# Kernel optimization log

Hardware: AMD Instinct MI355X
Metric: run time of the kernel (lower is better)

Reference implementation:

```python
import jax, jax.numpy as jnp
import numpy as np

SIZE, NC, BITS = 16, 3, 8
NV = NC * BITS * SIZE * SIZE  # 6144
NH = NV
N = 32
K_LS = 32   # fixed cap on T=0 local-search Gibbs sweeps (converged rows are fixed points)
K_CP = 16   # fixed cap on coupling MH iterations (converged rows masked out)


def float2bit(x, bits=BITS):
    # quantize [0,1) floats to `bits` binary planes, as in float2bit(...).flatten(1)
    q = jnp.clip(jnp.floor(x * (2 ** bits)), 0, 2 ** bits - 1).astype(jnp.int32)
    shifts = jnp.arange(bits, dtype=jnp.int32)
    b = (q[..., None] >> shifts) & 1  # [N,nc,H,W,bits]
    return b.astype(jnp.float32)


def energy(params, v, h0, h1):
    W0, W1, b0, b1, b2 = params
    e = -jnp.sum(v * b0, axis=1)
    e = e - jnp.sum(h0 * (v @ W0.T + b1), axis=1)
    e = e - jnp.sum(h1 * (h0 @ W1.T + b2), axis=1)
    return e


def _samp(logits, r, T):
    if T == 0:
        return (logits >= 0).astype(jnp.float32)
    return (r < jax.nn.sigmoid(logits / T)).astype(jnp.float32)


def gibbs_step(params, v, h0, h1, even, fix_v, T, key):
    W0, W1, b0, b1, b2 = params
    if T == 0:
        rv = rh0 = rh1 = None
    else:
        kv, k0, k1 = jax.random.split(key, 3)
        rv = jax.random.uniform(kv, v.shape)
        rh0 = jax.random.uniform(k0, h0.shape)
        rh1 = jax.random.uniform(k1, h1.shape)
    # 'even' sweep order: v -> odd h layers -> even h layers
    v_e = v if fix_v else _samp(h0 @ W0 + b0, rv, T)
    h1_e = _samp(h0 @ W1.T + b2, rh1, T)
    h0_e = _samp(v_e @ W0.T + b1 + h1_e @ W1, rh0, T)
    # 'odd' sweep order: even h layers -> v -> odd h layers
    h0_o = _samp(v @ W0.T + b1 + h1 @ W1, rh0, T)
    v_o = v if fix_v else _samp(h0_o @ W0 + b0, rv, T)
    h1_o = _samp(h0_o @ W1.T + b2, rh1, T)
    m = even[:, None]
    return (jnp.where(m, v_e, v_o), jnp.where(m, h0_e, h0_o), jnp.where(m, h1_e, h1_o))


def local_search(params, v, h0, h1, fix_v, key):
    # T=0 deterministic descent with a fixed per-row even/odd split (rand_u drawn once);
    # converged rows are fixed points of the map, so running a fixed K_LS sweeps over the
    # full batch is equivalent to the torch masked while-loop (up to the iteration cap).
    even = jax.random.uniform(key, (v.shape[0],)) < 0.5
    def body(i, s):
        return gibbs_step(params, s[0], s[1], s[2], even, fix_v, 0, None)
    return jax.lax.fori_loop(0, K_LS, body, (v, h0, h1))


def mh_step(params, v, h0, h1, fix_v, key):
    kv, k0, k1, ku = jax.random.split(key, 4)
    v_p = v if fix_v else (jax.random.uniform(kv, v.shape) < 0.5).astype(jnp.float32)
    h0_p = (jax.random.uniform(k0, h0.shape) < 0.5).astype(jnp.float32)
    h1_p = (jax.random.uniform(k1, h1.shape) < 0.5).astype(jnp.float32)
    log_ratio = energy(params, v, h0, h1) - energy(params, v_p, h0_p, h1_p)
    acc = jax.random.uniform(ku, (v.shape[0],)) < jnp.exp(jnp.minimum(log_ratio, 0.0))
    a = acc[:, None]
    return (v if fix_v else jnp.where(a, v_p, v), jnp.where(a, h0_p, h0), jnp.where(a, h1_p, h1))


def _conv_mask(v_new, h0_new, h1_new, v, h0, h1, fix_v):
    c = jnp.ones(v.shape[0], bool) if fix_v else jnp.all(v_new == v, axis=1)
    return c & jnp.all(h0_new == h0, axis=1) & jnp.all(h1_new == h1, axis=1)


def coupling(params, v, h0, h1, fix_v, key):
    k0, key = jax.random.split(key)
    v1, h01, h11 = mh_step(params, v, h0, h1, fix_v, k0)
    e = energy(params, v1, h01, h11)
    conv = _conv_mask(v1, h01, h11, v, h0, h1, fix_v)
    def body(state, k):
        v, h0, h1, e, conv = state
        v2, h02, h12 = mh_step(params, v, h0, h1, fix_v, k)
        de = energy(params, v2, h02, h12) - energy(params, v, h0, h1)
        m = ~conv
        e = e + jnp.where(m, de, 0.0)
        conv2 = _conv_mask(v2, h02, h12, v, h0, h1, fix_v)
        mm = m[:, None]
        v = jnp.where(mm, v2, v)
        h0 = jnp.where(mm, h02, h0)
        h1 = jnp.where(mm, h12, h1)
        return (v, h0, h1, e, conv | conv2), None
    keys = jax.random.split(key, K_CP)
    (v, h0, h1, e, conv), _ = jax.lax.scan(body, (v1, h01, h11, e, conv), keys)
    return e, v, h0, h1


def _dbm_loss(v_img, W0, W1, b0, b1, b2):
    params = (W0, W1, b0, b1, b2)
    n = v_img.shape[0]
    ks = jax.random.split(jax.random.key(42), 13)
    v = float2bit(v_img).reshape(n, -1)
    # positive phase (visibles clamped, fix_v=True)
    h0 = (jax.random.uniform(ks[0], (n, NH)) < 0.5).astype(jnp.float32)
    h1 = (jax.random.uniform(ks[1], (n, NH)) < 0.5).astype(jnp.float32)
    v, h0, h1 = local_search(params, v, h0, h1, True, ks[2])
    even = jax.random.uniform(ks[3], (n,)) < 0.5
    v, h0, h1 = gibbs_step(params, v, h0, h1, even, True, 1, ks[4])
    e_pos, v, h0, h1 = coupling(params, v, h0, h1, True, ks[5])
    # negative phase (free-running)
    v = (jax.random.uniform(ks[6], v.shape) < 0.5).astype(jnp.float32)
    h0 = (jax.random.uniform(ks[7], (n, NH)) < 0.5).astype(jnp.float32)
    h1 = (jax.random.uniform(ks[8], (n, NH)) < 0.5).astype(jnp.float32)
    v, h0, h1 = local_search(params, v, h0, h1, False, ks[9])
    even = jax.random.uniform(ks[10], (n,)) < 0.5
    v, h0, h1 = gibbs_step(params, v, h0, h1, even, False, 1, ks[11])
    e_neg, v, h0, h1 = coupling(params, v, h0, h1, False, ks[12])
    return e_pos - e_neg  # [N]


def setup_inputs() -> dict:
    key = jax.random.key(0)
    kv, kw0, kw1 = jax.random.split(key, 3)
    v = jax.random.uniform(kv, (N, NC, SIZE, SIZE), dtype=jnp.float32)
    # orthogonal-like scale (unit-norm rows): entries ~ 1/sqrt(fan_in)
    W0 = jax.random.normal(kw0, (NH, NV), dtype=jnp.float32) / np.sqrt(NV)
    W1 = jax.random.normal(kw1, (NH, NH), dtype=jnp.float32) / np.sqrt(NH)
    b0 = jnp.zeros((NV,), jnp.float32)
    b1 = jnp.zeros((NH,), jnp.float32)
    b2 = jnp.zeros((NH,), jnp.float32)
    return {"v": v, "W0": W0, "W1": W1, "b0": b0, "b1": b1, "b2": b2}


def reference(v, W0, W1, b0, b1, b2):
    return _dbm_loss(v, W0, W1, b0, b1, b2)
```

## Files before the change

kernel.cpp:

```cpp
#include <hip/hip_runtime.h>
#include <cstdint>
#include <math.h>

typedef unsigned int u32;
typedef unsigned long long u64;
typedef double d4 __attribute__((ext_vector_type(4)));

#define TF_PARTITIONABLE 1

#define NU 6144
#define NB 32
#define NTOT (NU * NB)
#define NWORD 96
#define SW (NB * NWORD)
#define NCH 16
#define CHK 384
#define NT_TILES 12
#define HALF_BIG 98304u
#define HALF_SMALL 16u

struct Key { u32 a, b; };
struct UVec { float u[NB]; };

__host__ __device__ __forceinline__ void tf2x32(u32 k0, u32 k1, u32 x0, u32 x1, u32& o0, u32& o1) {
  const u32 k2 = k0 ^ k1 ^ 0x1BD11BDAu;
#define TFR(r) { x0 += x1; x1 = (x1 << r) | (x1 >> (32 - r)); x1 ^= x0; }
  x0 += k0; x1 += k1;
  TFR(13) TFR(15) TFR(26) TFR(6)  x0 += k1; x1 += k2 + 1u;
  TFR(17) TFR(29) TFR(16) TFR(24) x0 += k2; x1 += k0 + 2u;
  TFR(13) TFR(15) TFR(26) TFR(6)  x0 += k0; x1 += k1 + 3u;
  TFR(17) TFR(29) TFR(16) TFR(24) x0 += k1; x1 += k2 + 4u;
  TFR(13) TFR(15) TFR(26) TFR(6)  x0 += k2; x1 += k0 + 5u;
#undef TFR
  o0 = x0; o1 = x1;
}

__host__ __device__ __forceinline__ u32 rbits(u32 k0, u32 k1, u32 t, u32 half) {
#if TF_PARTITIONABLE
  (void)half;
  u32 a, b; tf2x32(k0, k1, 0u, t, a, b); return a ^ b;
#else
  u32 a, b;
  if (t < half) { tf2x32(k0, k1, t, half + t, a, b); return a; }
  tf2x32(k0, k1, t - half, t, a, b); return b;
#endif
}

__host__ __device__ __forceinline__ float u01f(u32 bits) {
  union { u32 u; float f; } c; c.u = (bits >> 9) | 0x3f800000u;
  return c.f - 1.0f;
}

__device__ __forceinline__ double pav(int probe, int l) {
  return probe ? (double)(((l * 13 + 5) & 63) + 1) : (double)(l + 1);
}
__device__ __forceinline__ double pbv(int probe, int l) {
  return probe ? (double)(((l * 11 + 2) & 63) + 1) : (double)(((l * 7 + 3) & 63) + 1);
}

__global__ __launch_bounds__(64) void k_calib(int* __restrict__ tbl) {
  int L = threadIdx.x;
  d4 z = {0.0, 0.0, 0.0, 0.0};
  d4 o0 = __builtin_amdgcn_mfma_f64_16x16x4f64(pav(0, L), pbv(0, L), z, 0, 0, 0);
  d4 o1 = __builtin_amdgcn_mfma_f64_16x16x4f64(pav(1, L), pbv(1, L), z, 0, 0, 0);
  int q = L >> 4, m16 = L & 15;
  int best = -1;
  for (int combo = 0; combo < 16; ++combo) {
    int fa = combo & 1, fb = (combo >> 1) & 1, fd = combo >> 2;
    int ok = 1;
    for (int probe = 0; probe < 2; ++probe) {
#pragma unroll
      for (int r = 0; r < 4; ++r) {
        int i, j;
        if (fd == 0)      { j = m16; i = 4 * q + r; }
        else if (fd == 1) { j = m16; i = q + 4 * r; }
        else if (fd == 2) { i = m16; j = 4 * q + r; }
        else              { i = m16; j = q + 4 * r; }
        double pred = 0.0;
#pragma unroll
        for (int k = 0; k < 4; ++k) {
          int la = fa ? (i * 4 + k) : (k * 16 + i);
          int lb = fb ? (j * 4 + k) : (k * 16 + j);
          pred += pav(probe, la) * pbv(probe, lb);
        }
        double obs = probe ? (r == 0 ? o1[0] : r == 1 ? o1[1] : r == 2 ? o1[2] : o1[3])
                           : (r == 0 ? o0[0] : r == 1 ? o0[1] : r == 2 ? o0[2] : o0[3]);
        if (pred != obs) ok = 0;
      }
    }
    if (__all(ok) && best < 0) best = combo;
  }
  int mA = 0, kA = 0, nB = 0, kB = 0, b0_ = 0, bs = 0, j0 = 0, js = 0, okf = 0;
  if (best >= 0) {
    int fa = best & 1, fb = (best >> 1) & 1, fd = best >> 2;
    if (fa) { mA = L >> 2; kA = L & 3; } else { mA = m16; kA = q; }
    if (fb) { nB = L >> 2; kB = L & 3; } else { nB = m16; kB = q; }
    if (fd == 0)      { j0 = m16; js = 0; b0_ = 4 * q; bs = 1; }
    else if (fd == 1) { j0 = m16; js = 0; b0_ = q; bs = 4; }
    else if (fd == 2) { b0_ = m16; bs = 0; j0 = 4 * q; js = 1; }
    else              { b0_ = m16; bs = 0; j0 = q; js = 4; }
    okf = 1;
  }
  int* p = tbl + L * 16;
  p[0] = mA; p[1] = kA; p[2] = nB; p[3] = kB;
  p[4] = b0_; p[5] = bs; p[6] = j0; p[7] = js; p[8] = okf;
}

__global__ void k_init(u32* __restrict__ a, u32* __restrict__ b) { *a = 0u; *b = 0u; }

__global__ void k_allconv(const u32* __restrict__ conv, u32* __restrict__ skipc) {
  if (*skipc) return;
  u32 all = 1u;
  for (int b = 0; b < NB; ++b) all &= conv[b];
  if (all) *skipc = 1u;
}

__global__ __launch_bounds__(256) void k_cyc(const u64* __restrict__ s0, const u64* __restrict__ s1,
                                             const u64* __restrict__ s2, u64* __restrict__ save,
                                             int slot, int docmp, int rem_odd, int prev_slot,
                                             u32* __restrict__ flag, u32* __restrict__ fix) {
  if (*flag) return;
  __shared__ u32 neq_sh;
  if (threadIdx.x == 0) neq_sh = 0u;
  __syncthreads();
  u64* sp = save + (size_t)slot * (3 * SW);
  u32 neq = 0;
  for (int w = threadIdx.x; w < SW; w += 256) {
    u64 a0 = s0[w]; if (a0 != sp[w]) neq = 1; sp[w] = a0;
    u64 a1 = s1[w]; if (a1 != sp[SW + w]) neq = 1; sp[SW + w] = a1;
    if (s2) { u64 a2 = s2[w]; if (a2 != sp[2 * SW + w]) neq = 1; sp[2 * SW + w] = a2; }
  }
  if (neq) neq_sh = 1u;
  __syncthreads();
  if (threadIdx.x == 0 && docmp && neq_sh == 0u) {
    *flag = 1u;
    *fix = rem_odd ? (1u + (u32)prev_slot) : 0u;
  }
}

__global__ __launch_bounds__(256) void k_fixup(u64* __restrict__ s0, u64* __restrict__ s1,
                                               u64* __restrict__ s2, const u64* __restrict__ save,
                                               const u32* __restrict__ flag, const u32* __restrict__ fix) {
  if (!*flag || !*fix) return;
  const u64* sp = save + (size_t)(*fix - 1u) * (3 * SW);
  int w = blockIdx.x * 256 + threadIdx.x;
  if (w < SW) {
    s0[w] = sp[w];
    s1[w] = sp[SW + w];
    if (s2) s2[w] = sp[2 * SW + w];
  }
}

__global__ __launch_bounds__(256) void k_pos_v(const float* __restrict__ vin, u64* __restrict__ pk) {
  int tid = blockIdx.x * 256 + threadIdx.x;
  int b = tid / 768, p = tid % 768;
  float x = vin[tid];
  int q = (int)floorf(x * 256.0f);
  q = q < 0 ? 0 : (q > 255 ? 255 : q);
  ((unsigned char*)pk)[b * 768 + p] = (unsigned char)q;
}

__global__ __launch_bounds__(256) void k_bern(u32 k0, u32 k1, u64* __restrict__ pk) {
  int tid = blockIdx.x * 256 + threadIdx.x;
  bool s = u01f(rbits(k0, k1, (u32)tid, HALF_BIG)) < 0.5f;
  u64 m = __ballot(s);
  if ((threadIdx.x & 63) == 0) pk[tid >> 6] = m;
}

__global__ __launch_bounds__(256) void k_bern3(u32 has_v, u32 va, u32 vb, u32 ha0, u32 hb0,
                                               u32 ha1, u32 hb1,
                                               u64* __restrict__ pkv, u64* __restrict__ pkh0,
                                               u64* __restrict__ pkh1, const u32* __restrict__ skip) {
  if (skip && *skip) return;
  int tid = blockIdx.x * 256 + threadIdx.x;
  int lane0 = (threadIdx.x & 63) == 0;
  if (has_v) {
    bool s = u01f(rbits(va, vb, (u32)tid, HALF_BIG)) < 0.5f;
    u64 m = __ballot(s);
    if (lane0) pkv[tid >> 6] = m;
  }
  { bool s = u01f(rbits(ha0, hb0, (u32)tid, HALF_BIG)) < 0.5f;
    u64 m = __ballot(s);
    if (lane0) pkh0[tid >> 6] = m; }
  { bool s = u01f(rbits(ha1, hb1, (u32)tid, HALF_BIG)) < 0.5f;
    u64 m = __ballot(s);
    if (lane0) pkh1[tid >> 6] = m; }
}

__device__ __forceinline__ bool samp_dec(float f, int t1, u32 k0, u32 k1, u32 tid) {
  if (t1) {
    double u = (double)u01f(rbits(k0, k1, tid, HALF_BIG));
    return u < 1.0 / (1.0 + exp(-(double)f));
  }
  return f >= 0.0f;
}

__global__ __launch_bounds__(256) void k_samp(const float* __restrict__ fE, const float* __restrict__ fO,
                                              u32 even, int t1, u32 k0, u32 k1,
                                              u64* __restrict__ pk, const u32* __restrict__ skip) {
  if (skip && *skip) return;
  int tid = blockIdx.x * 256 + threadIdx.x;
  int b = tid / NU;
  float f = ((even >> b) & 1u) ? fE[tid] : fO[tid];
  bool s = samp_dec(f, t1, k0, k1, (u32)tid);
  u64 m = __ballot(s);
  if ((threadIdx.x & 63) == 0) pk[tid >> 6] = m;
}

__global__ __launch_bounds__(256) void k_gemm_n(const float* __restrict__ W, const u64* __restrict__ pkx,
                                                double* __restrict__ part, const u32* __restrict__ skip,
                                                const int* __restrict__ tbl) {
  if (skip && *skip) return;
  __shared__ double smem_d[2560];
  int jt = blockIdx.x % 96, c = blockIdx.x / 96;
  int wid = threadIdx.x >> 6, lane = threadIdx.x & 63;
  int kbase = c * CHK;
  int jn0 = jt * 64;
  const int* tp = tbl + lane * 16;
  int okf = tp[8];
  if (okf) {
    float* lw = (float*)smem_d;
    int mA = tp[0], kA = tp[1], nB = tp[2], kB = tp[3];
    int bD0 = tp[4], bDs = tp[5], jD0 = tp[6], jDs = tp[7];
    int t256 = threadIdx.x;
    d4 acc0 = {0.0, 0.0, 0.0, 0.0};
    d4 acc1 = {0.0, 0.0, 0.0, 0.0};
#pragma unroll
    for (int r = 0; r < 2; ++r) {
      int idx = r * 256 + t256, kk = idx >> 4, qq = idx & 15;
      float4 w4 = *(const float4*)(W + (size_t)(kbase + kk) * NU + jn0 + 4 * qq);
      float* d = &lw[kk * 80 + 4 * qq];
      d[0] = w4.x; d[1] = w4.y; d[2] = w4.z; d[3] = w4.w;
    }
    __syncthreads();
    const u64* pxr0 = pkx + (size_t)mA * NWORD + (kbase >> 6);
    const u64* pxr1 = pkx + (size_t)(mA + 16) * NWORD + (kbase >> 6);
    int buf = 0;
    for (int t = 0; t < NT_TILES; ++t) {
      float4 w0p, w1p;
      bool pf = (t + 1) < NT_TILES;
      if (pf) {
        int k0n = kbase + (t + 1) * 32;
        { int idx = t256,       kk = idx >> 4, qq = idx & 15;
          w0p = *(const float4*)(W + (size_t)(k0n + kk) * NU + jn0 + 4 * qq); }
        { int idx = 256 + t256, kk = idx >> 4, qq = idx & 15;
          w1p = *(const float4*)(W + (size_t)(k0n + kk) * NU + jn0 + 4 * qq); }
      }
      u64 ww0 = pxr0[t >> 1], ww1 = pxr1[t >> 1];
      u32 sh = ((u32)(t & 1) << 5) + (u32)kA;
      u32 bb0 = (u32)(ww0 >> sh), bb1 = (u32)(ww1 >> sh);
      const float* lwp = &lw[(buf * 32 + kB) * 80 + wid * 16 + nB];
#pragma unroll
      for (int u = 0; u < 8; ++u) {
        double a0 = (double)((bb0 >> (4 * u)) & 1u);
        double a1 = (double)((bb1 >> (4 * u)) & 1u);
        double wv = (double)lwp[320 * u];
        acc0 = __builtin_amdgcn_mfma_f64_16x16x4f64(a0, wv, acc0, 0, 0, 0);
        acc1 = __builtin_amdgcn_mfma_f64_16x16x4f64(a1, wv, acc1, 0, 0, 0);
      }
      if (pf) {
        int nb = buf ^ 1;
        { int idx = t256,       kk = idx >> 4, qq = idx & 15;
          float* d = &lw[(nb * 32 + kk) * 80 + 4 * qq];
          d[0] = w0p.x; d[1] = w0p.y; d[2] = w0p.z; d[3] = w0p.w; }
        { int idx = 256 + t256, kk = idx >> 4, qq = idx & 15;
          float* d = &lw[(nb * 32 + kk) * 80 + 4 * qq];
          d[0] = w1p.x; d[1] = w1p.y; d[2] = w1p.z; d[3] = w1p.w; }
      }
      __syncthreads();
      buf ^= 1;
    }
    int jn = jn0 + wid * 16;
    double* pp = part + (size_t)c * NTOT + jn;
#pragma unroll
    for (int r = 0; r < 4; ++r) {
      int bi = bD0 + bDs * r, jj = jD0 + jDs * r;
      pp[(size_t)bi * NU + jj] = acc0[r];
      pp[(size_t)(bi + 16) * NU + jj] = acc1[r];
    }
  } else {
    double* red = smem_d;
    int j = jn0 + lane;
    int i0 = kbase + wid * (CHK / 4);
    const float* wp = W + (size_t)i0 * NU + j;
    for (int g = 0; g < 4; ++g) {
      double acc[8];
#pragma unroll
      for (int b = 0; b < 8; ++b) acc[b] = 0.0;
      for (int i = 0; i < CHK / 4; ++i) {
        double w = (double)wp[(size_t)i * NU];
        int k = i0 + i;
#pragma unroll
        for (int b = 0; b < 8; ++b) {
          double xb = (double)((pkx[(size_t)(g * 8 + b) * NWORD + (k >> 6)] >> (k & 63)) & 1ull);
          acc[b] = fma(xb, w, acc[b]);
        }
      }
      for (int w2 = 1; w2 < 4; ++w2) {
        if (wid == w2) {
#pragma unroll
          for (int b = 0; b < 8; ++b) red[b * 64 + lane] = acc[b];
        }
        __syncthreads();
        if (wid == 0) {
#pragma unroll
          for (int b = 0; b < 8; ++b) acc[b] += red[b * 64 + lane];
        }
        __syncthreads();
      }
      if (wid == 0) {
        double* pp = part + (size_t)c * NTOT + j;
#pragma unroll
        for (int b = 0; b < 8; ++b) pp[(size_t)(g * 8 + b) * NU] = acc[b];
      }
      __syncthreads();
    }
  }
}

__global__ __launch_bounds__(256) void k_gemm_t(const float* __restrict__ W, const u64* __restrict__ pkx,
                                                double* __restrict__ part, const u32* __restrict__ skip,
                                                const int* __restrict__ tbl) {
  if (skip && *skip) return;
  __shared__ double smem_d[2176];
  int jt = blockIdx.x % 96, c = blockIdx.x / 96;
  int wid = threadIdx.x >> 6, lane = threadIdx.x & 63;
  int kbase = c * CHK;
  int jn0 = jt * 64;
  const int* tp = tbl + lane * 16;
  int okf = tp[8];
  if (okf) {
    float* lw = (float*)smem_d;
    int mA = tp[0], kA = tp[1], nB = tp[2], kB = tp[3];
    int bD0 = tp[4], bDs = tp[5], jD0 = tp[6], jDs = tp[7];
    int t256 = threadIdx.x;
    d4 acc0 = {0.0, 0.0, 0.0, 0.0};
    d4 acc1 = {0.0, 0.0, 0.0, 0.0};
#pragma unroll
    for (int r = 0; r < 2; ++r) {
      int idx = r * 256 + t256, jj = idx >> 3, kq = idx & 7;
      float4 w4 = *(const float4*)(W + (size_t)(jn0 + jj) * NU + kbase + 4 * kq);
      float* d = &lw[jj * 34 + 4 * kq];
      d[0] = w4.x; d[1] = w4.y; d[2] = w4.z; d[3] = w4.w;
    }
    __syncthreads();
    const u64* pxr0 = pkx + (size_t)mA * NWORD + (kbase >> 6);
    const u64* pxr1 = pkx + (size_t)(mA + 16) * NWORD + (kbase >> 6);
    int buf = 0;
    for (int t = 0; t < NT_TILES; ++t) {
      float4 w0p, w1p;
      bool pf = (t + 1) < NT_TILES;
      if (pf) {
        int k0n = kbase + (t + 1) * 32;
        { int idx = t256,       jj = idx >> 3, kq = idx & 7;
          w0p = *(const float4*)(W + (size_t)(jn0 + jj) * NU + k0n + 4 * kq); }
        { int idx = 256 + t256, jj = idx >> 3, kq = idx & 7;
          w1p = *(const float4*)(W + (size_t)(jn0 + jj) * NU + k0n + 4 * kq); }
      }
      u64 ww0 = pxr0[t >> 1], ww1 = pxr1[t >> 1];
      u32 sh = ((u32)(t & 1) << 5) + (u32)kA;
      u32 bb0 = (u32)(ww0 >> sh), bb1 = (u32)(ww1 >> sh);
      const float* lwp = &lw[(buf * 64 + wid * 16 + nB) * 34 + kB];
#pragma unroll
      for (int u = 0; u < 8; ++u) {
        double a0 = (double)((bb0 >> (4 * u)) & 1u);
        double a1 = (double)((bb1 >> (4 * u)) & 1u);
        double wv = (double)lwp[4 * u];
        acc0 = __builtin_amdgcn_mfma_f64_16x16x4f64(a0, wv, acc0, 0, 0, 0);
        acc1 = __builtin_amdgcn_mfma_f64_16x16x4f64(a1, wv, acc1, 0, 0, 0);
      }
      if (pf) {
        int nb = buf ^ 1;
        { int idx = t256,       jj = idx >> 3, kq = idx & 7;
          float* d = &lw[(nb * 64 + jj) * 34 + 4 * kq];
          d[0] = w0p.x; d[1] = w0p.y; d[2] = w0p.z; d[3] = w0p.w; }
        { int idx = 256 + t256, jj = idx >> 3, kq = idx & 7;
          float* d = &lw[(nb * 64 + jj) * 34 + 4 * kq];
          d[0] = w1p.x; d[1] = w1p.y; d[2] = w1p.z; d[3] = w1p.w; }
      }
      __syncthreads();
      buf ^= 1;
    }
    int jn = jn0 + wid * 16;
    double* pp = part + (size_t)c * NTOT + jn;
#pragma unroll
    for (int r = 0; r < 4; ++r) {
      int bi = bD0 + bDs * r, jj = jD0 + jDs * r;
      pp[(size_t)bi * NU + jj] = acc0[r];
      pp[(size_t)(bi + 16) * NU + jj] = acc1[r];
    }
  } else {
    float* lwf = (float*)smem_d;
    double* red = smem_d;
    int qf = threadIdx.x & 7, af = threadIdx.x >> 3;
    for (int g = 0; g < 4; ++g) {
      double acc[8];
#pragma unroll
      for (int b = 0; b < 8; ++b) acc[b] = 0.0;
      for (int s = 0; s < NT_TILES; ++s) {
        int ib = kbase + s * 32;
#pragma unroll
        for (int pass = 0; pass < 2; ++pass) {
          int r = pass * 32 + af;
          float4 w4 = *(const float4*)(W + (size_t)(jn0 + r) * NU + ib + qf * 4);
          lwf[(qf * 4 + 0) * 65 + r] = w4.x;
          lwf[(qf * 4 + 1) * 65 + r] = w4.y;
          lwf[(qf * 4 + 2) * 65 + r] = w4.z;
          lwf[(qf * 4 + 3) * 65 + r] = w4.w;
        }
        __syncthreads();
        int iw = wid * 8;
        for (int ii = 0; ii < 8; ++ii) {
          double w = (double)lwf[(iw + ii) * 65 + lane];
          int k = ib + iw + ii;
#pragma unroll
          for (int b = 0; b < 8; ++b) {
            double xb = (double)((pkx[(size_t)(g * 8 + b) * NWORD + (k >> 6)] >> (k & 63)) & 1ull);
            acc[b] = fma(xb, w, acc[b]);
          }
        }
        __syncthreads();
      }
      for (int w2 = 1; w2 < 4; ++w2) {
        if (wid == w2) {
#pragma unroll
          for (int b = 0; b < 8; ++b) red[b * 64 + lane] = acc[b];
        }
        __syncthreads();
        if (wid == 0) {
#pragma unroll
          for (int b = 0; b < 8; ++b) acc[b] += red[b * 64 + lane];
        }
        __syncthreads();
      }
      if (wid == 0) {
        double* pp = part + (size_t)c * NTOT + jn0 + lane;
#pragma unroll
        for (int b = 0; b < 8; ++b) pp[(size_t)(g * 8 + b) * NU] = acc[b];
      }
      __syncthreads();
    }
  }
}

__global__ __launch_bounds__(256) void k_reduce(const double* __restrict__ part, const float* __restrict__ bias,
                                                const float* __restrict__ src, float* __restrict__ out,
                                                const u32* __restrict__ skip) {
  if (skip && *skip) return;
  int tid = blockIdx.x * 256 + threadIdx.x;
  int j = tid % NU;
  double s = src ? (double)src[tid] : 0.0;
  if (bias) s += (double)bias[j];
#pragma unroll
  for (int c = 0; c < NCH; ++c) s += part[(size_t)c * NTOT + tid];
  out[tid] = (float)s;
}

__global__ __launch_bounds__(256) void k_redsamp(const double* __restrict__ part, const float* __restrict__ bias,
                                                 const float* __restrict__ src, float* __restrict__ out,
                                                 int t1, u32 k0, u32 k1,
                                                 u64* __restrict__ pk,
                                                 const u32* __restrict__ skip, u32 wmask) {
  if (skip && *skip) return;
  int tid = blockIdx.x * 256 + threadIdx.x;
  int j = tid % NU, b = tid / NU;
  double s = src ? (double)src[tid] : 0.0;
  if (bias) s += (double)bias[j];
#pragma unroll
  for (int c = 0; c < NCH; ++c) s += part[(size_t)c * NTOT + tid];
  float f = (float)s;
  if (out) out[tid] = f;
  bool wr = (wmask >> b) & 1u;
  bool smp = samp_dec(f, t1, k0, k1, (u32)tid);
  u64 m = __ballot(smp);
  if (((threadIdx.x & 63) == 0) && wr) pk[tid >> 6] = m;
  (void)j;
}

__global__ __launch_bounds__(256) void k_energy(const u64* __restrict__ pkv, const u64* __restrict__ pkh0,
                                                const u64* __restrict__ pkh1, const float* __restrict__ f1,
                                                const float* __restrict__ f2, const float* __restrict__ b0,
                                                float* __restrict__ eout, const u32* __restrict__ skip) {
  if (skip && *skip) return;
  __shared__ double red[256];
  int b = blockIdx.x, t = threadIdx.x;
  double s = 0.0;
  for (int j = t; j < NU; j += 256) {
    int w = j >> 6, bit = j & 63;
    if ((pkv [b * NWORD + w] >> bit) & 1ull) s += (double)b0[j];
    if ((pkh0[b * NWORD + w] >> bit) & 1ull) s += (double)f1[(size_t)b * NU + j];
    if ((pkh1[b * NWORD + w] >> bit) & 1ull) s += (double)f2[(size_t)b * NU + j];
  }
  red[t] = s; __syncthreads();
  for (int off = 128; off > 0; off >>= 1) { if (t < off) red[t] += red[t + off]; __syncthreads(); }
  if (t == 0) eout[b] = (float)(-red[0]);
}

__global__ __launch_bounds__(64) void k_accept(float* __restrict__ ecur, const float* __restrict__ eprop,
                                               float* __restrict__ erun, u32* __restrict__ conv,
                                               u32* __restrict__ accf,
                                               const u64* __restrict__ pv, const u64* __restrict__ pcv,
                                               const u64* __restrict__ ph0, const u64* __restrict__ pch0,
                                               const u64* __restrict__ ph1, const u64* __restrict__ pch1,
                                               UVec uv, int first, const u32* __restrict__ skip) {
  if (skip && *skip) return;
  int b = blockIdx.x, t = threadIdx.x;
  u64 diff = 0ull;
  for (int w = t; w < NWORD; w += 64) {
    size_t o = (size_t)b * NWORD + w;
    if (pv) diff |= pv[o] ^ pcv[o];
    diff |= ph0[o] ^ pch0[o];
    diff |= ph1[o] ^ pch1[o];
  }
  int neq = __any(diff != 0ull);
  if (t == 0) {
    float ec = ecur[b], ep = eprop[b];
    bool acc = (double)uv.u[b] < exp(fmin((double)ec - (double)ep, 0.0));
    bool m = first ? true : (conv[b] == 0u);
    bool upd = m && acc;
    if (first) erun[b] = acc ? ep : ec;
    else if (upd) erun[b] += (ep - ec);
    if (upd) ecur[b] = ep;
    u32 c2 = acc ? (neq ? 0u : 1u) : 1u;
    conv[b] = first ? c2 : (conv[b] | c2);
    accf[b] = upd ? 1u : 0u;
  }
}

__global__ __launch_bounds__(256) void k_merge_pk(const u32* __restrict__ accf,
                                                  const u64* __restrict__ pa, u64* __restrict__ ca,
                                                  const u64* __restrict__ pb, u64* __restrict__ cb,
                                                  const u64* __restrict__ pc, u64* __restrict__ cc,
                                                  const u32* __restrict__ skip) {
  if (skip && *skip) return;
  int w = blockIdx.x * 256 + threadIdx.x;
  if (w >= NB * NWORD) return;
  int b = w / NWORD;
  if (accf[b]) {
    ca[w] = pa[w];
    cb[w] = pb[w];
    if (pc) cc[w] = pc[w];
  }
}

__global__ void k_final(const float* __restrict__ ep, const float* __restrict__ en, float* __restrict__ out) {
  int b = threadIdx.x;
  if (b < NB) out[b] = ep[b] - en[b];
}

static void split_keys(Key k, int n, Key* out) {
#if TF_PARTITIONABLE
  for (int i = 0; i < n; ++i) { u32 a, b; tf2x32(k.a, k.b, 0u, (u32)i, a, b); out[i].a = a; out[i].b = b; }
#else
  u32 flat[64];
  for (int i = 0; i < n; ++i) { u32 a, b; tf2x32(k.a, k.b, (u32)i, (u32)(n + i), a, b); flat[i] = a; flat[n + i] = b; }
  for (int i = 0; i < n; ++i) { out[i].a = flat[2 * i]; out[i].b = flat[2 * i + 1]; }
#endif
}
static u32 mask32(Key k) {
  u32 m = 0;
  for (int b = 0; b < NB; ++b)
    if (u01f(rbits(k.a, k.b, (u32)b, HALF_SMALL)) < 0.5f) m |= (1u << b);
  return m;
}

extern "C" void kernel_launch(void* const* d_in, const int* in_sizes, int n_in,
                              void* d_out, int out_size, void* d_ws, size_t ws_size,
                              hipStream_t stream) {
  const float* vin = (const float*)d_in[0];
  const float* W0  = (const float*)d_in[1];
  const float* W1  = (const float*)d_in[2];
  const float* b0  = (const float*)d_in[3];
  const float* b1  = (const float*)d_in[4];
  const float* b2  = (const float*)d_in[5];
  float* outp = (float*)d_out;

  char* ws = (char*)d_ws;
  size_t off = 0;
  auto alloc = [&](size_t bytes) -> void* {
    void* p = ws + off; off += (bytes + 255) & ~(size_t)255; return p;
  };
  enum { SV = 0, SH0, SH1, SVE, SH1E, SH0O, SVP, SH0P, SH1P, NS };
  enum { IV = 0, IA, IB, IC, ID, IE, IF2, NF };
  u64* PK[NS]; float* F[NF];
  for (int f = 0; f < NF; ++f) F[f] = (float*)alloc((size_t)NTOT * 4);
  double* PART = (double*)alloc((size_t)NCH * NTOT * 8);
  for (int s = 0; s < NS; ++s) PK[s] = (u64*)alloc((size_t)NB * NWORD * 8);
  u64*   SAVE   = (u64*)alloc((size_t)2 * 3 * SW * 8);
  int*   TBL    = (int*)alloc(64 * 16 * 4);
  float* E_CUR  = (float*)alloc(256);
  float* E_PROP = (float*)alloc(256);
  float* E_POS  = (float*)alloc(256);
  float* E_NEG  = (float*)alloc(256);
  u32*   ACC    = (u32*)alloc(256);
  u32*   CONV   = (u32*)alloc(256);
  u32*   FLAG   = (u32*)alloc(256);
  u32*   FIX    = (u32*)alloc(256);
  u32*   SKIPC  = (u32*)alloc(256);
  u32*   DUMMY  = (u32*)alloc(256);
  if (off > ws_size) return;

  Key root{0u, 42u};
  Key ks[13]; split_keys(root, 13, ks);
  const Key KZ{0u, 0u};

  k_calib<<<dim3(1), dim3(64), 0, stream>>>(TBL);

  auto GEMM_T = [&](const float* Wm, int xs, const u32* skip) {
    k_gemm_t<<<dim3(96 * NCH), dim3(256), 0, stream>>>(Wm, PK[xs], PART, skip, TBL);
  };
  auto GEMM_N = [&](const float* Wm, int xs, const u32* skip) {
    k_gemm_n<<<dim3(96 * NCH), dim3(256), 0, stream>>>(Wm, PK[xs], PART, skip, TBL);
  };
  auto RED = [&](const float* bias, const float* src, float* dst, const u32* skip) {
    k_reduce<<<dim3(768), dim3(256), 0, stream>>>(PART, bias, src, dst, skip);
  };
  auto REDS = [&](const float* bias, const float* src, float* dst, int t1, Key k, int sdst,
                  const u32* skip, u32 wm) {
    k_redsamp<<<dim3(768), dim3(256), 0, stream>>>(PART, bias, src, dst, t1, k.a, k.b,
                                                   PK[sdst], skip, wm);
  };
  auto GT = [&](const float* Wm, int xs, const float* bias, const float* src, float* dst, const u32* skip) {
    GEMM_T(Wm, xs, skip); RED(bias, src, dst, skip);
  };
  auto GN = [&](const float* Wm, int xs, const float* bias, const float* src, float* dst, const u32* skip) {
    GEMM_N(Wm, xs, skip); RED(bias, src, dst, skip);
  };
  auto GTS = [&](const float* Wm, int xs, const float* bias, const float* src, float* dst,
                 int t1, Key k, int sdst, const u32* skip) {
    GEMM_T(Wm, xs, skip); REDS(bias, src, dst, t1, k, sdst, skip, ~0u);
  };
  auto GNS = [&](const float* Wm, int xs, const float* bias, const float* src, float* dst,
                 int t1, Key k, int sdst, const u32* skip) {
    GEMM_N(Wm, xs, skip); REDS(bias, src, dst, t1, k, sdst, skip, ~0u);
  };
  auto SAMP = [&](const float* fE, const float* fO, u32 even, int t1, Key k, int dst) {
    k_samp<<<dim3(768), dim3(256), 0, stream>>>(fE, fO, even, t1, k.a, k.b, PK[dst], nullptr);
  };
  auto BERN = [&](Key k, int dst) {
    k_bern<<<dim3(768), dim3(256), 0, stream>>>(k.a, k.b, PK[dst]);
  };
  auto ENERGY = [&](int sv, int sh0, int sh1, const float* f1, const float* f2, float* eo, const u32* skip) {
    k_energy<<<dim3(32), dim3(256), 0, stream>>>(PK[sv], PK[sh0], PK[sh1], f1, f2, b0, eo, skip);
  };

  auto ls_fixv = [&](u32 evm) {
    auto X = [&](u32 wm, const u32* skip) {
      GEMM_T(W1, SH0, skip);
      REDS(b2, nullptr, nullptr, 0, KZ, SH1, skip, wm);
    };
    auto Y = [&](const u32* skip) {
      GEMM_N(W1, SH1, skip);
      REDS(nullptr, F[IV], nullptr, 0, KZ, SH0, skip, ~0u);
    };
    k_init<<<dim3(1), dim3(1), 0, stream>>>(FLAG, FIX);
    X(evm, nullptr);
    for (int i = 1; i <= 31; ++i) {
      Y(FLAG); X(~0u, FLAG);
      k_cyc<<<dim3(1), dim3(256), 0, stream>>>(PK[SH0], PK[SH1], nullptr, SAVE,
          i & 1, (i >= 3) ? 1 : 0, (31 - i) & 1, (i - 1) & 1, FLAG, FIX);
    }
    k_fixup<<<dim3(12), dim3(256), 0, stream>>>(PK[SH0], PK[SH1], nullptr, SAVE, FLAG, FIX);
    Y(nullptr); X(~evm, nullptr);
  };
  auto ls_free = [&](u32 evm) {
    auto X = [&](u32 wm, const u32* skip) {
      GEMM_N(W0, SH0, skip);
      REDS(b0, nullptr, nullptr, 0, KZ, SV, skip, wm);
      GEMM_T(W1, SH0, skip);
      REDS(b2, nullptr, nullptr, 0, KZ, SH1, skip, wm);
    };
    auto Y = [&](const u32* skip) {
      GT(W0, SV, b1, nullptr, F[IC], skip);
      GEMM_N(W1, SH1, skip);
      REDS(nullptr, F[IC], nullptr, 0, KZ, SH0, skip, ~0u);
    };
    k_init<<<dim3(1), dim3(1), 0, stream>>>(FLAG, FIX);
    X(evm, nullptr);
    for (int i = 1; i <= 31; ++i) {
      Y(FLAG); X(~0u, FLAG);
      k_cyc<<<dim3(1), dim3(256), 0, stream>>>(PK[SV], PK[SH0], PK[SH1], SAVE,
          i & 1, (i >= 3) ? 1 : 0, (31 - i) & 1, (i - 1) & 1, FLAG, FIX);
    }
    k_fixup<<<dim3(12), dim3(256), 0, stream>>>(PK[SV], PK[SH0], PK[SH1], SAVE, FLAG, FIX);
    Y(nullptr); X(~evm, nullptr);
  };

  auto gibbs_fixv = [&](u32 even, Key kh0, Key kh1) {
    GTS(W1, SH0, b2, nullptr, F[IA], 1, kh1, SH1E, nullptr);
    GN(W1, SH1E, nullptr, F[IV], F[IB], nullptr);
    GNS(W1, SH1, nullptr, F[IV], F[IC], 1, kh0, SH0O, nullptr);
    GT(W1, SH0O, b2, nullptr, F[ID], nullptr);
    SAMP(F[IB], F[IC], even, 1, kh0, SH0);
    SAMP(F[IA], F[ID], even, 1, kh1, SH1);
  };
  auto gibbs_free = [&](u32 even, Key kv, Key kh0, Key kh1) {
    GNS(W0, SH0, b0, nullptr, F[IE], 1, kv, SVE, nullptr);
    GTS(W1, SH0, b2, nullptr, F[IA], 1, kh1, SH1E, nullptr);
    GT(W0, SVE, b1, nullptr, F[IB], nullptr);
    GN(W1, SH1E, nullptr, F[IB], F[IB], nullptr);
    GT(W0, SV, b1, nullptr, F[IC], nullptr);
    GNS(W1, SH1, nullptr, F[IC], F[IC], 1, kh0, SH0O, nullptr);
    GN(W0, SH0O, b0, nullptr, F[IF2], nullptr);
    GT(W1, SH0O, b2, nullptr, F[ID], nullptr);
    SAMP(F[IE], F[IF2], even, 1, kv, SV);
    SAMP(F[IB], F[IC], even, 1, kh0, SH0);
    SAMP(F[IA], F[ID], even, 1, kh1, SH1);
  };

  auto coupling = [&](bool fixv, Key ck, float* erun) {
    Key top[2]; split_keys(ck, 2, top);
    Key cks[17]; cks[0] = top[0];
    { Key rest[16]; split_keys(top[1], 16, rest); for (int i = 0; i < 16; ++i) cks[i + 1] = rest[i]; }
    k_init<<<dim3(1), dim3(1), 0, stream>>>(SKIPC, DUMMY);
    for (int it = 0; it < 17; ++it) {
      const u32* sk = (it == 0) ? nullptr : SKIPC;
      Key sub[4]; split_keys(cks[it], 4, sub);
      UVec uv;
      for (int b = 0; b < NB; ++b) uv.u[b] = u01f(rbits(sub[3].a, sub[3].b, (u32)b, HALF_SMALL));
      k_bern3<<<dim3(768), dim3(256), 0, stream>>>(fixv ? 0u : 1u,
          sub[0].a, sub[0].b, sub[1].a, sub[1].b, sub[2].a, sub[2].b,
          PK[SVP], PK[SH0P], PK[SH1P], sk);
      const float* f1;
      if (fixv) f1 = F[IV];
      else { GT(W0, SVP, b1, nullptr, F[IC], sk); f1 = F[IC]; }
      GT(W1, SH0P, b2, nullptr, F[ID], sk);
      ENERGY(fixv ? SV : SVP, SH0P, SH1P, f1, F[ID], E_PROP, sk);
      k_accept<<<dim3(32), dim3(64), 0, stream>>>(E_CUR, E_PROP, erun, CONV, ACC,
          fixv ? nullptr : PK[SVP], fixv ? nullptr : PK[SV],
          PK[SH0P], PK[SH0], PK[SH1P], PK[SH1], uv, it == 0 ? 1 : 0, sk);
      k_merge_pk<<<dim3(12), dim3(256), 0, stream>>>(ACC, PK[SH0P], PK[SH0], PK[SH1P], PK[SH1],
          fixv ? nullptr : PK[SVP], fixv ? nullptr : PK[SV], sk);
      k_allconv<<<dim3(1), dim3(1), 0, stream>>>(CONV, SKIPC);
    }
  };

  k_pos_v<<<dim3(96), dim3(256), 0, stream>>>(vin, PK[SV]);
  BERN(ks[0], SH0);
  BERN(ks[1], SH1);
  GT(W0, SV, b1, nullptr, F[IV], nullptr);
  u32 ev_ls_pos = mask32(ks[2]);
  ls_fixv(ev_ls_pos);
  u32 ev2_pos = mask32(ks[3]);
  Key g4[3]; split_keys(ks[4], 3, g4);
  gibbs_fixv(ev2_pos, g4[1], g4[2]);
  GT(W1, SH0, b2, nullptr, F[ID], nullptr);
  ENERGY(SV, SH0, SH1, F[IV], F[ID], E_CUR, nullptr);
  coupling(true, ks[5], E_POS);

  BERN(ks[6], SV);
  BERN(ks[7], SH0);
  BERN(ks[8], SH1);
  u32 ev_ls_neg = mask32(ks[9]);
  ls_free(ev_ls_neg);
  u32 ev2_neg = mask32(ks[10]);
  Key g11[3]; split_keys(ks[11], 3, g11);
  gibbs_free(ev2_neg, g11[0], g11[1], g11[2]);
  GT(W0, SV, b1, nullptr, F[IB], nullptr);
  GT(W1, SH0, b2, nullptr, F[IA], nullptr);
  ENERGY(SV, SH0, SH1, F[IB], F[IA], E_CUR, nullptr);
  coupling(false, ks[12], E_NEG);

  k_final<<<dim3(1), dim3(64), 0, stream>>>(E_POS, E_NEG, outp);
}
```

Baseline: 13.70 ms.

## Load GEMM weights directly into registers instead of staging through LDS

Both binary-activation GEMM kernels stop staging W tiles in double-buffered shared memory and read each lane's MFMA operands straight from global memory, with a one-tile register prefetch. The packed bit words are preloaded into registers. In the transposed kernel the k-to-lane mapping changes so each lane reads 8 contiguous floats as two float4 loads. The fallback paths drop the cross-wave LDS reduction by giving each wave its own 8 batch rows. This removes the __syncthreads barriers and LDS traffic, at the cost of less coalesced global loads and no data sharing between waves.

```diff
diff --git a/kernel.cpp b/kernel.cpp
--- a/kernel.cpp
+++ b/kernel.cpp
@@ -211,7 +211,6 @@
                                                 double* __restrict__ part, const u32* __restrict__ skip,
                                                 const int* __restrict__ tbl) {
   if (skip && *skip) return;
-  __shared__ double smem_d[2560];
   int jt = blockIdx.x % 96, c = blockIdx.x / 96;
   int wid = threadIdx.x >> 6, lane = threadIdx.x & 63;
   int kbase = c * CHK;
@@ -219,56 +218,37 @@
   const int* tp = tbl + lane * 16;
   int okf = tp[8];
   if (okf) {
-    float* lw = (float*)smem_d;
     int mA = tp[0], kA = tp[1], nB = tp[2], kB = tp[3];
     int bD0 = tp[4], bDs = tp[5], jD0 = tp[6], jDs = tp[7];
-    int t256 = threadIdx.x;
     d4 acc0 = {0.0, 0.0, 0.0, 0.0};
     d4 acc1 = {0.0, 0.0, 0.0, 0.0};
-#pragma unroll
-    for (int r = 0; r < 2; ++r) {
-      int idx = r * 256 + t256, kk = idx >> 4, qq = idx & 15;
-      float4 w4 = *(const float4*)(W + (size_t)(kbase + kk) * NU + jn0 + 4 * qq);
-      float* d = &lw[kk * 80 + 4 * qq];
-      d[0] = w4.x; d[1] = w4.y; d[2] = w4.z; d[3] = w4.w;
-    }
-    __syncthreads();
-    const u64* pxr0 = pkx + (size_t)mA * NWORD + (kbase >> 6);
-    const u64* pxr1 = pkx + (size_t)(mA + 16) * NWORD + (kbase >> 6);
-    int buf = 0;
+    const u64* px0 = pkx + (size_t)mA * NWORD + (kbase >> 6);
+    const u64* px1 = pkx + (size_t)(mA + 16) * NWORD + (kbase >> 6);
+    u64 xw0[6], xw1[6];
+#pragma unroll
+    for (int i = 0; i < 6; ++i) { xw0[i] = px0[i]; xw1[i] = px1[i]; }
+    const float* wb = W + (size_t)(kbase + kB) * NU + jn0 + wid * 16 + nB;
+    float cur[8], nxt[8];
+#pragma unroll
+    for (int u = 0; u < 8; ++u) cur[u] = wb[(size_t)(4 * u) * NU];
     for (int t = 0; t < NT_TILES; ++t) {
-      float4 w0p, w1p;
-      bool pf = (t + 1) < NT_TILES;
-      if (pf) {
-        int k0n = kbase + (t + 1) * 32;
-        { int idx = t256,       kk = idx >> 4, qq = idx & 15;
-          w0p = *(const float4*)(W + (size_t)(k0n + kk) * NU + jn0 + 4 * qq); }
-        { int idx = 256 + t256, kk = idx >> 4, qq = idx & 15;
-          w1p = *(const float4*)(W + (size_t)(k0n + kk) * NU + jn0 + 4 * qq); }
+      if (t + 1 < NT_TILES) {
+        const float* wn = wb + (size_t)((t + 1) * 32) * NU;
+#pragma unroll
+        for (int u = 0; u < 8; ++u) nxt[u] = wn[(size_t)(4 * u) * NU];
       }
-      u64 ww0 = pxr0[t >> 1], ww1 = pxr1[t >> 1];
-      u32 sh = ((u32)(t & 1) << 5) + (u32)kA;
-      u32 bb0 = (u32)(ww0 >> sh), bb1 = (u32)(ww1 >> sh);
-      const float* lwp = &lw[(buf * 32 + kB) * 80 + wid * 16 + nB];
+      u32 bb0 = (u32)(xw0[t >> 1] >> (((t & 1) << 5) + kA));
+      u32 bb1 = (u32)(xw1[t >> 1] >> (((t & 1) << 5) + kA));
 #pragma unroll
       for (int u = 0; u < 8; ++u) {
+        double wv = (double)cur[u];
         double a0 = (double)((bb0 >> (4 * u)) & 1u);
         double a1 = (double)((bb1 >> (4 * u)) & 1u);
-        double wv = (double)lwp[320 * u];
         acc0 = __builtin_amdgcn_mfma_f64_16x16x4f64(a0, wv, acc0, 0, 0, 0);
         acc1 = __builtin_amdgcn_mfma_f64_16x16x4f64(a1, wv, acc1, 0, 0, 0);
       }
-      if (pf) {
-        int nb = buf ^ 1;
-        { int idx = t256,       kk = idx >> 4, qq = idx & 15;
-          float* d = &lw[(nb * 32 + kk) * 80 + 4 * qq];
-          d[0] = w0p.x; d[1] = w0p.y; d[2] = w0p.z; d[3] = w0p.w; }
-        { int idx = 256 + t256, kk = idx >> 4, qq = idx & 15;
-          float* d = &lw[(nb * 32 + kk) * 80 + 4 * qq];
-          d[0] = w1p.x; d[1] = w1p.y; d[2] = w1p.z; d[3] = w1p.w; }
-      }
-      __syncthreads();
-      buf ^= 1;
+#pragma unroll
+      for (int u = 0; u < 8; ++u) cur[u] = nxt[u];
     }
     int jn = jn0 + wid * 16;
     double* pp = part + (size_t)c * NTOT + jn;
@@ -279,42 +259,23 @@
       pp[(size_t)(bi + 16) * NU + jj] = acc1[r];
     }
   } else {
-    double* red = smem_d;
     int j = jn0 + lane;
-    int i0 = kbase + wid * (CHK / 4);
-    const float* wp = W + (size_t)i0 * NU + j;
-    for (int g = 0; g < 4; ++g) {
-      double acc[8];
-#pragma unroll
-      for (int b = 0; b < 8; ++b) acc[b] = 0.0;
-      for (int i = 0; i < CHK / 4; ++i) {
-        double w = (double)wp[(size_t)i * NU];
-        int k = i0 + i;
-#pragma unroll
-        for (int b = 0; b < 8; ++b) {
-          double xb = (double)((pkx[(size_t)(g * 8 + b) * NWORD + (k >> 6)] >> (k & 63)) & 1ull);
-          acc[b] = fma(xb, w, acc[b]);
-        }
+    const float* wp = W + (size_t)kbase * NU + j;
+    double acc[8];
+#pragma unroll
+    for (int b = 0; b < 8; ++b) acc[b] = 0.0;
+    for (int i = 0; i < CHK; ++i) {
+      double w = (double)wp[(size_t)i * NU];
+      int k = kbase + i;
+#pragma unroll
+      for (int b = 0; b < 8; ++b) {
+        double xb = (double)((pkx[(size_t)(wid * 8 + b) * NWORD + (k >> 6)] >> (k & 63)) & 1ull);
+        acc[b] = fma(xb, w, acc[b]);
       }
-      for (int w2 = 1; w2 < 4; ++w2) {
-        if (wid == w2) {
-#pragma unroll
-          for (int b = 0; b < 8; ++b) red[b * 64 + lane] = acc[b];
-        }
-        __syncthreads();
-        if (wid == 0) {
-#pragma unroll
-          for (int b = 0; b < 8; ++b) acc[b] += red[b * 64 + lane];
-        }
-        __syncthreads();
-      }
-      if (wid == 0) {
-        double* pp = part + (size_t)c * NTOT + j;
-#pragma unroll
-        for (int b = 0; b < 8; ++b) pp[(size_t)(g * 8 + b) * NU] = acc[b];
-      }
-      __syncthreads();
-    }
+    }
+    double* pp = part + (size_t)c * NTOT + j;
+#pragma unroll
+    for (int b = 0; b < 8; ++b) pp[(size_t)(wid * 8 + b) * NU] = acc[b];
   }
 }
 
@@ -322,7 +283,6 @@
                                                 double* __restrict__ part, const u32* __restrict__ skip,
                                                 const int* __restrict__ tbl) {
   if (skip && *skip) return;
-  __shared__ double smem_d[2176];
   int jt = blockIdx.x % 96, c = blockIdx.x / 96;
   int wid = threadIdx.x >> 6, lane = threadIdx.x & 63;
   int kbase = c * CHK;
@@ -330,56 +290,40 @@
   const int* tp = tbl + lane * 16;
   int okf = tp[8];
   if (okf) {
-    float* lw = (float*)smem_d;
     int mA = tp[0], kA = tp[1], nB = tp[2], kB = tp[3];
     int bD0 = tp[4], bDs = tp[5], jD0 = tp[6], jDs = tp[7];
-    int t256 = threadIdx.x;
     d4 acc0 = {0.0, 0.0, 0.0, 0.0};
     d4 acc1 = {0.0, 0.0, 0.0, 0.0};
-#pragma unroll
-    for (int r = 0; r < 2; ++r) {
-      int idx = r * 256 + t256, jj = idx >> 3, kq = idx & 7;
-      float4 w4 = *(const float4*)(W + (size_t)(jn0 + jj) * NU + kbase + 4 * kq);
-      float* d = &lw[jj * 34 + 4 * kq];
-      d[0] = w4.x; d[1] = w4.y; d[2] = w4.z; d[3] = w4.w;
-    }
-    __syncthreads();
-    const u64* pxr0 = pkx + (size_t)mA * NWORD + (kbase >> 6);
-    const u64* pxr1 = pkx + (size_t)(mA + 16) * NWORD + (kbase >> 6);
-    int buf = 0;
+    const u64* px0 = pkx + (size_t)mA * NWORD + (kbase >> 6);
+    const u64* px1 = pkx + (size_t)(mA + 16) * NWORD + (kbase >> 6);
+    u64 xw0[6], xw1[6];
+#pragma unroll
+    for (int i = 0; i < 6; ++i) { xw0[i] = px0[i]; xw1[i] = px1[i]; }
+    const float* wb = W + (size_t)(jn0 + wid * 16 + nB) * NU + kbase + kB * 8;
+    float4 c0 = *(const float4*)(wb);
+    float4 c1 = *(const float4*)(wb + 4);
     for (int t = 0; t < NT_TILES; ++t) {
-      float4 w0p, w1p;
-      bool pf = (t + 1) < NT_TILES;
-      if (pf) {
-        int k0n = kbase + (t + 1) * 32;
-        { int idx = t256,       jj = idx >> 3, kq = idx & 7;
-          w0p = *(const float4*)(W + (size_t)(jn0 + jj) * NU + k0n + 4 * kq); }
-        { int idx = 256 + t256, jj = idx >> 3, kq = idx & 7;
-          w1p = *(const float4*)(W + (size_t)(jn0 + jj) * NU + k0n + 4 * kq); }
+      float4 n0, n1;
+      if (t + 1 < NT_TILES) {
+        const float* wn = wb + (t + 1) * 32;
+        n0 = *(const float4*)(wn);
+        n1 = *(const float4*)(wn + 4);
       }
-      u64 ww0 = pxr0[t >> 1], ww1 = pxr1[t >> 1];
-      u32 sh = ((u32)(t & 1) << 5) + (u32)kA;
-      u32 bb0 = (u32)(ww0 >> sh), bb1 = (u32)(ww1 >> sh);
-      const float* lwp = &lw[(buf * 64 + wid * 16 + nB) * 34 + kB];
+      u32 bb0 = (u32)(xw0[t >> 1] >> (((t & 1) << 5) + kA * 8));
+      u32 bb1 = (u32)(xw1[t >> 1] >> (((t & 1) << 5) + kA * 8));
+      float fr0 = c0.x, fr1 = c0.y, fr2 = c0.z, fr3 = c0.w;
+      float fr4 = c1.x, fr5 = c1.y, fr6 = c1.z, fr7 = c1.w;
 #pragma unroll
       for (int u = 0; u < 8; ++u) {
-        double a0 = (double)((bb0 >> (4 * u)) & 1u);
-        double a1 = (double)((bb1 >> (4 * u)) & 1u);
-        double wv = (double)lwp[4 * u];
+        float fv = (u == 0) ? fr0 : (u == 1) ? fr1 : (u == 2) ? fr2 : (u == 3) ? fr3
+                 : (u == 4) ? fr4 : (u == 5) ? fr5 : (u == 6) ? fr6 : fr7;
+        double wv = (double)fv;
+        double a0 = (double)((bb0 >> u) & 1u);
+        double a1 = (double)((bb1 >> u) & 1u);
         acc0 = __builtin_amdgcn_mfma_f64_16x16x4f64(a0, wv, acc0, 0, 0, 0);
         acc1 = __builtin_amdgcn_mfma_f64_16x16x4f64(a1, wv, acc1, 0, 0, 0);
       }
-      if (pf) {
-        int nb = buf ^ 1;
-        { int idx = t256,       jj = idx >> 3, kq = idx & 7;
-          float* d = &lw[(nb * 64 + jj) * 34 + 4 * kq];
-          d[0] = w0p.x; d[1] = w0p.y; d[2] = w0p.z; d[3] = w0p.w; }
-        { int idx = 256 + t256, jj = idx >> 3, kq = idx & 7;
-          float* d = &lw[(nb * 64 + jj) * 34 + 4 * kq];
-          d[0] = w1p.x; d[1] = w1p.y; d[2] = w1p.z; d[3] = w1p.w; }
-      }
-      __syncthreads();
-      buf ^= 1;
+      c0 = n0; c1 = n1;
     }
     int jn = jn0 + wid * 16;
     double* pp = part + (size_t)c * NTOT + jn;
@@ -390,56 +334,23 @@
       pp[(size_t)(bi + 16) * NU + jj] = acc1[r];
     }
   } else {
-    float* lwf = (float*)smem_d;
-    double* red = smem_d;
-    int qf = threadIdx.x & 7, af = threadIdx.x >> 3;
-    for (int g = 0; g < 4; ++g) {
-      double acc[8];
-#pragma unroll
-      for (int b = 0; b < 8; ++b) acc[b] = 0.0;
-      for (int s = 0; s < NT_TILES; ++s) {
-        int ib = kbase + s * 32;
-#pragma unroll
-        for (int pass = 0; pass < 2; ++pass) {
-          int r = pass * 32 + af;
-          float4 w4 = *(const float4*)(W + (size_t)(jn0 + r) * NU + ib + qf * 4);
-          lwf[(qf * 4 + 0) * 65 + r] = w4.x;
-          lwf[(qf * 4 + 1) * 65 + r] = w4.y;
-          lwf[(qf * 4 + 2) * 65 + r] = w4.z;
-          lwf[(qf * 4 + 3) * 65 + r] = w4.w;
-        }
-        __syncthreads();
-        int iw = wid * 8;
-        for (int ii = 0; ii < 8; ++ii) {
-          double w = (double)lwf[(iw + ii) * 65 + lane];
-          int k = ib + iw + ii;
-#pragma unroll
-          for (int b = 0; b < 8; ++b) {
-            double xb = (double)((pkx[(size_t)(g * 8 + b) * NWORD + (k >> 6)] >> (k & 63)) & 1ull);
-            acc[b] = fma(xb, w, acc[b]);
-          }
-        }
-        __syncthreads();
+    int j = jn0 + lane;
+    const float* wp = W + (size_t)j * NU + kbase;
+    double acc[8];
+#pragma unroll
+    for (int b = 0; b < 8; ++b) acc[b] = 0.0;
+    for (int i = 0; i < CHK; ++i) {
+      double w = (double)wp[i];
+      int k = kbase + i;
+#pragma unroll
+      for (int b = 0; b < 8; ++b) {
+        double xb = (double)((pkx[(size_t)(wid * 8 + b) * NWORD + (k >> 6)] >> (k & 63)) & 1ull);
+        acc[b] = fma(xb, w, acc[b]);
       }
-      for (int w2 = 1; w2 < 4; ++w2) {
-        if (wid == w2) {
-#pragma unroll
-          for (int b = 0; b < 8; ++b) red[b * 64 + lane] = acc[b];
-        }
-        __syncthreads();
-        if (wid == 0) {
-#pragma unroll
-          for (int b = 0; b < 8; ++b) acc[b] += red[b * 64 + lane];
-        }
-        __syncthreads();
-      }
-      if (wid == 0) {
-        double* pp = part + (size_t)c * NTOT + jn0 + lane;
-#pragma unroll
-        for (int b = 0; b < 8; ++b) pp[(size_t)(g * 8 + b) * NU] = acc[b];
-      }
-      __syncthreads();
-    }
+    }
+    double* pp = part + (size_t)c * NTOT + j;
+#pragma unroll
+    for (int b = 0; b < 8; ++b) pp[(size_t)(wid * 8 + b) * NU] = acc[b];
   }
 }
 
```

Result: faster. 12.70 ms (-7.3%).
